# Performance work log

Hardware: AMD Instinct MI355X
Metric: run time of the kernel (lower is better)

## Reference

```python
import jax, jax.numpy as jnp
import numpy as np

TEMPERATURE = 0.07
SCALE_BY_TEMPERATURE = True
N = 4096
D = 256
N_POS = 32768
CHUNK = 128  # row-chunk size for the cdist to bound the [CHUNK, N, D] temp


def setup_inputs() -> dict:
    key = jax.random.key(0)
    k1, k2, k3 = jax.random.split(key, 3)
    out = jax.random.normal(k1, (N, D), dtype=jnp.float32)
    row = jax.random.randint(k2, (N_POS,), 0, N, dtype=jnp.int32)
    col = jax.random.randint(k3, (N_POS,), 0, N, dtype=jnp.int32)
    return {"out": out, "row": row, "col": col}


def _l1_cdist(x):
    """Pairwise Manhattan distance [N, N], computed in row chunks so the
    [CHUNK, N, D] broadcast temporary stays bounded."""
    n, d = x.shape
    xr = x.reshape(n // CHUNK, CHUNK, d)

    def chunk_dist(xc):  # xc: [CHUNK, D] -> [CHUNK, N]
        return jnp.sum(jnp.abs(xc[:, None, :] - x[None, :, :]), axis=-1)

    return jax.lax.map(chunk_dist, xr).reshape(n, n)


def reference(out, row, col):
    n = out.shape[0]
    sim = -_l1_cdist(out) / TEMPERATURE                      # [N, N]
    logits_max = jax.lax.stop_gradient(jnp.max(sim, axis=1, keepdims=True))
    sim = sim - logits_max
    logits_mask = 1.0 - jnp.eye(n, dtype=sim.dtype)          # zero out self-sims
    denom = jnp.log(jnp.sum(jnp.exp(sim) * logits_mask, axis=1, keepdims=True))
    log_probs = sim - denom                                  # [N, N]
    loss = -jnp.mean(log_probs[row, col])                    # gather positive pairs
    if SCALE_BY_TEMPERATURE:
        loss = loss * TEMPERATURE
    return loss
```

## Files before the change

kernel.cpp:

```cpp
#include <hip/hip_runtime.h>
#include <math.h>

#define N 4096
#define D 256
#define NPOS 32768
#define TEMP 0.07f
#define INVT (1.0f / 0.07f)
#define BIGF 3.0e38f

#define RQ 5.5f
#define QS (255.0f / (2.0f * RQ))
#define DEQ (2.0f * RQ / 255.0f)

#define NT 64
#define NTRI (NT * (NT + 1) / 2)
#define KC 16
#define LP 68

#define WS_PSTAT 0
#define WS_T    (2 * N * NT)
#define WS_ACC  (2 * N * NT + N)
#define WS_CNT  (2 * N * NT + N + 1)
#define WS_XQ   (2 * N * NT + N + 4)

__device__ __forceinline__ void sad_acc(unsigned a, unsigned b, unsigned& c) {
#if __has_builtin(__builtin_amdgcn_sad_u8)
    c = __builtin_amdgcn_sad_u8(a, b, c);
#else
    asm("v_sad_u8 %0, %1, %2, %0" : "+v"(c) : "v"(a), "v"(b));
#endif
}

__device__ __forceinline__ unsigned quant1(float v) {
    const float f = fminf(fmaxf((v + RQ) * QS, 0.0f), 255.0f);
    return (unsigned)__float2uint_rn(f);
}

__global__ __launch_bounds__(256)
void cvt_init_k(const float* __restrict__ x, unsigned* __restrict__ xq,
                float* __restrict__ acc, unsigned* __restrict__ cnt) {
    const int i = blockIdx.x * 256 + threadIdx.x;
    const float4 v = ((const float4*)x)[i];
    const unsigned q = quant1(v.x) | (quant1(v.y) << 8) |
                       (quant1(v.z) << 16) | (quant1(v.w) << 24);
    xq[i] = q;
    if (i == 0) { *acc = 0.0f; *cnt = 0u; }
}

__global__ __launch_bounds__(64, 2)
void dist_tile_k(const unsigned* __restrict__ xq, float2* __restrict__ pstat) {
    const int tt = blockIdx.x;
    const int u_ = (NTRI - 1) - tt;
    int r = (int)((sqrtf((float)(8 * u_ + 1)) - 1.0f) * 0.5f);
    while (r * (r + 1) / 2 > u_) --r;
    while ((r + 1) * (r + 2) / 2 <= u_) ++r;
    const int bm = (NT - 1) - r;
    const int bn = (NT - 1) - (u_ - r * (r + 1) / 2);
    const bool diag = (bm == bn);

    const int lane = threadIdx.x;
    const int tx = lane & 7;
    const int ty = lane >> 3;

    __shared__ unsigned As[KC][LP];
    __shared__ unsigned Bs[KC][LP];

    unsigned uacc[2][2][4][4];
#pragma unroll
    for (int rh = 0; rh < 2; ++rh)
#pragma unroll
        for (int ch = 0; ch < 2; ++ch)
#pragma unroll
            for (int i = 0; i < 4; ++i)
#pragma unroll
                for (int j = 0; j < 4; ++j) uacc[rh][ch][i][j] = 0u;

    const int rowA0 = bm * 64;
    const int rowB0 = bn * 64;

    const int su = lane & 3;
    const int r0 = lane >> 2;
    const uint4* gA = (const uint4*)xq + (size_t)(rowA0 + r0) * 16 + su;
    const uint4* gB = (const uint4*)xq + (size_t)(rowB0 + r0) * 16 + su;

    const int aoff = ty * 4;
    const int boff = tx * 4;

    for (int chk = 0; chk < 4; ++chk) {
        uint4 la[4], lb[4];
#pragma unroll
        for (int c = 0; c < 4; ++c) la[c] = gA[chk * 4 + (size_t)c * 256];
#pragma unroll
        for (int c = 0; c < 4; ++c) lb[c] = gB[chk * 4 + (size_t)c * 256];
        asm volatile("s_waitcnt lgkmcnt(0)" ::: "memory");
#pragma unroll
        for (int c = 0; c < 4; ++c) {
            const int rr = r0 + 16 * c;
            As[su * 4 + 0][rr] = la[c].x; As[su * 4 + 1][rr] = la[c].y;
            As[su * 4 + 2][rr] = la[c].z; As[su * 4 + 3][rr] = la[c].w;
            Bs[su * 4 + 0][rr] = lb[c].x; Bs[su * 4 + 1][rr] = lb[c].y;
            Bs[su * 4 + 2][rr] = lb[c].z; Bs[su * 4 + 3][rr] = lb[c].w;
        }
        asm volatile("s_waitcnt lgkmcnt(0)" ::: "memory");

#pragma unroll
        for (int k4 = 0; k4 < KC; ++k4) {
            const uint4 alo = *(const uint4*)&As[k4][aoff];
            const uint4 ahi = *(const uint4*)&As[k4][aoff + 32];
            const uint4 blo = *(const uint4*)&Bs[k4][boff];
            const uint4 bhi = *(const uint4*)&Bs[k4][boff + 32];
            const unsigned av[2][4] = {{alo.x, alo.y, alo.z, alo.w},
                                       {ahi.x, ahi.y, ahi.z, ahi.w}};
            const unsigned bv[2][4] = {{blo.x, blo.y, blo.z, blo.w},
                                       {bhi.x, bhi.y, bhi.z, bhi.w}};
#pragma unroll
            for (int rh = 0; rh < 2; ++rh)
#pragma unroll
                for (int chq = 0; chq < 2; ++chq)
#pragma unroll
                    for (int i = 0; i < 4; ++i)
#pragma unroll
                        for (int j = 0; j < 4; ++j)
                            sad_acc(av[rh][i], bv[chq][j], uacc[rh][chq][i][j]);
        }
    }

    float acc[2][2][4][4];
#pragma unroll
    for (int rh = 0; rh < 2; ++rh)
#pragma unroll
        for (int chq = 0; chq < 2; ++chq)
#pragma unroll
            for (int i = 0; i < 4; ++i)
#pragma unroll
                for (int j = 0; j < 4; ++j)
                    acc[rh][chq][i][j] = (float)uacc[rh][chq][i][j] * DEQ;

    if (diag) {
#pragma unroll
        for (int rh = 0; rh < 2; ++rh)
#pragma unroll
            for (int chq = 0; chq < 2; ++chq)
#pragma unroll
                for (int i = 0; i < 4; ++i)
#pragma unroll
                    for (int j = 0; j < 4; ++j)
                        if (rh * 32 + ty * 4 + i == chq * 32 + tx * 4 + j)
                            acc[rh][chq][i][j] = BIGF;
    }

#pragma unroll
    for (int rh = 0; rh < 2; ++rh) {
#pragma unroll
        for (int i = 0; i < 4; ++i) {
            float mn = BIGF;
#pragma unroll
            for (int chq = 0; chq < 2; ++chq)
#pragma unroll
                for (int j = 0; j < 4; ++j) mn = fminf(mn, acc[rh][chq][i][j]);
            mn = fminf(mn, __shfl_xor(mn, 1, 64));
            mn = fminf(mn, __shfl_xor(mn, 2, 64));
            mn = fminf(mn, __shfl_xor(mn, 4, 64));
            float s = 0.0f;
#pragma unroll
            for (int chq = 0; chq < 2; ++chq)
#pragma unroll
                for (int j = 0; j < 4; ++j)
                    s += __expf((mn - acc[rh][chq][i][j]) * INVT);
            s += __shfl_xor(s, 1, 64);
            s += __shfl_xor(s, 2, 64);
            s += __shfl_xor(s, 4, 64);
            if (tx == 0)
                pstat[(size_t)(rowA0 + rh * 32 + ty * 4 + i) * NT + bn] =
                    make_float2(mn, s);
        }
    }

    if (!diag) {
#pragma unroll
        for (int chq = 0; chq < 2; ++chq) {
#pragma unroll
            for (int j = 0; j < 4; ++j) {
                float mn = BIGF;
#pragma unroll
                for (int rh = 0; rh < 2; ++rh)
#pragma unroll
                    for (int i = 0; i < 4; ++i) mn = fminf(mn, acc[rh][chq][i][j]);
                mn = fminf(mn, __shfl_xor(mn, 8, 64));
                mn = fminf(mn, __shfl_xor(mn, 16, 64));
                mn = fminf(mn, __shfl_xor(mn, 32, 64));
                float s = 0.0f;
#pragma unroll
                for (int rh = 0; rh < 2; ++rh)
#pragma unroll
                    for (int i = 0; i < 4; ++i)
                        s += __expf((mn - acc[rh][chq][i][j]) * INVT);
                s += __shfl_xor(s, 8, 64);
                s += __shfl_xor(s, 16, 64);
                s += __shfl_xor(s, 32, 64);
                if (ty == 0)
                    pstat[(size_t)(rowB0 + chq * 32 + tx * 4 + j) * NT + bm] =
                        make_float2(mn, s);
            }
        }
    }
}

__global__ __launch_bounds__(256)
void row_stats_k(const float2* __restrict__ pstat, float* __restrict__ t) {
    const int r = blockIdx.x * 4 + (threadIdx.x >> 6);
    const int c = threadIdx.x & 63;
    const float2 p = pstat[(size_t)r * NT + c];
    float mn = p.x;
#pragma unroll
    for (int off = 32; off > 0; off >>= 1) mn = fminf(mn, __shfl_xor(mn, off, 64));
    float s = p.y * __expf((mn - p.x) * INVT);
#pragma unroll
    for (int off = 32; off > 0; off >>= 1) s += __shfl_xor(s, off, 64);
    if (c == 0) t[r] = TEMP * __logf(s) - mn;
}

__global__ __launch_bounds__(256)
void pair_fin_k(const float* __restrict__ x, const int* __restrict__ row,
                const int* __restrict__ col, const float* __restrict__ t,
                float* __restrict__ acc, unsigned* __restrict__ cnt,
                float* __restrict__ out) {
    const int lane = threadIdx.x & 63;
    const int wave = threadIdx.x >> 6;
    const int p0 = (blockIdx.x * 4 + wave) * 8;

    int rp[8], cp[8];
#pragma unroll
    for (int i = 0; i < 8; ++i) { rp[i] = row[p0 + i]; cp[i] = col[p0 + i]; }
    float4 a[8], b[8];
#pragma unroll
    for (int i = 0; i < 8; ++i) {
        a[i] = *(const float4*)&x[(size_t)rp[i] * D + lane * 4];
        b[i] = *(const float4*)&x[(size_t)cp[i] * D + lane * 4];
    }
    float wsum = 0.0f;
#pragma unroll
    for (int i = 0; i < 8; ++i) {
        float d = fabsf(a[i].x - b[i].x) + fabsf(a[i].y - b[i].y) +
                  fabsf(a[i].z - b[i].z) + fabsf(a[i].w - b[i].w);
#pragma unroll
        for (int off = 32; off > 0; off >>= 1) d += __shfl_xor(d, off, 64);
        if (lane == 0) wsum += d + t[rp[i]];
    }

    __shared__ float bs[4];
    if (lane == 0) bs[wave] = wsum;
    __syncthreads();
    if (threadIdx.x == 0) {
        const float tot = bs[0] + bs[1] + bs[2] + bs[3];
        atomicAdd(acc, tot);
        __threadfence();
        const unsigned tk = atomicAdd(cnt, 1u);
        if (tk == (unsigned)(gridDim.x - 1)) {
            const float v = atomicAdd(acc, 0.0f);
            out[0] = v * (1.0f / (float)NPOS);
        }
    }
}

extern "C" void kernel_launch(void* const* d_in, const int* in_sizes, int n_in,
                              void* d_out, int out_size, void* d_ws, size_t ws_size,
                              hipStream_t stream) {
    const float* x = (const float*)d_in[0];
    const int* row = (const int*)d_in[1];
    const int* col = (const int*)d_in[2];
    float* ws = (float*)d_ws;
    float* out = (float*)d_out;
    unsigned* xq = (unsigned*)(ws + WS_XQ);
    float* acc = ws + WS_ACC;
    unsigned* cnt = (unsigned*)(ws + WS_CNT);

    cvt_init_k<<<(N * D / 4) / 256, 256, 0, stream>>>(x, xq, acc, cnt);

    dist_tile_k<<<NTRI, 64, 0, stream>>>(xq, (float2*)(ws + WS_PSTAT));

    row_stats_k<<<N / 4, 256, 0, stream>>>((const float2*)(ws + WS_PSTAT), ws + WS_T);

    pair_fin_k<<<NPOS / 32, 256, 0, stream>>>(x, row, col, ws + WS_T, acc, cnt, out);
}
```

Measured before the change: 132.1 us.

## Split each 64x64 distance tile across two wavefronts with shared-memory row-stat merge

Each distance tile is now handled by a 128-thread block of two wavefronts. Each wave computes half of the tile's columns, so per-thread accumulators are halved and more waves can be resident per CU. The row min and sum-of-exp from the two waves are merged through shared memory before being written out. The price is __syncthreads barriers around every LDS staging step plus an extra merge pass, and the A-tile LDS reads are now duplicated across both waves.

Result: faster. 125.4 us, median of 2 (-5.0%).

```diff
diff --git a/kernel.cpp b/kernel.cpp
--- a/kernel.cpp
+++ b/kernel.cpp
@@ -47,7 +47,7 @@
     if (i == 0) { *acc = 0.0f; *cnt = 0u; }
 }
 
-__global__ __launch_bounds__(64, 2)
+__global__ __launch_bounds__(128, 4)
 void dist_tile_k(const unsigned* __restrict__ xq, float2* __restrict__ pstat) {
     const int tt = blockIdx.x;
     const int u_ = (NTRI - 1) - tt;
@@ -58,95 +58,89 @@
     const int bn = (NT - 1) - (u_ - r * (r + 1) / 2);
     const bool diag = (bm == bn);
 
-    const int lane = threadIdx.x;
+    const int tid = threadIdx.x;
+    const int lane = tid & 63;
+    const int w = tid >> 6;
     const int tx = lane & 7;
     const int ty = lane >> 3;
 
     __shared__ unsigned As[KC][LP];
     __shared__ unsigned Bs[KC][LP];
-
-    unsigned uacc[2][2][4][4];
+    __shared__ float rmin_s[2][64];
+    __shared__ float rsum_s[2][64];
+
+    unsigned uacc[2][4][4];
 #pragma unroll
     for (int rh = 0; rh < 2; ++rh)
 #pragma unroll
-        for (int ch = 0; ch < 2; ++ch)
-#pragma unroll
-            for (int i = 0; i < 4; ++i)
-#pragma unroll
-                for (int j = 0; j < 4; ++j) uacc[rh][ch][i][j] = 0u;
+        for (int i = 0; i < 4; ++i)
+#pragma unroll
+            for (int j = 0; j < 4; ++j) uacc[rh][i][j] = 0u;
 
     const int rowA0 = bm * 64;
     const int rowB0 = bn * 64;
 
-    const int su = lane & 3;
-    const int r0 = lane >> 2;
-    const uint4* gA = (const uint4*)xq + (size_t)(rowA0 + r0) * 16 + su;
-    const uint4* gB = (const uint4*)xq + (size_t)(rowB0 + r0) * 16 + su;
-
-    const int aoff = ty * 4;
-    const int boff = tx * 4;
+    const int sr = tid >> 2;
+    const int su = tid & 3;
+    const uint4* gA0 = (const uint4*)xq + (size_t)(rowA0 + sr) * 16 + su;
+    const uint4* gA1 = (const uint4*)xq + (size_t)(rowA0 + sr + 32) * 16 + su;
+    const uint4* gB0 = (const uint4*)xq + (size_t)(rowB0 + sr) * 16 + su;
+    const uint4* gB1 = (const uint4*)xq + (size_t)(rowB0 + sr + 32) * 16 + su;
+
+    const int boff = w * 32 + tx * 4;
 
     for (int chk = 0; chk < 4; ++chk) {
-        uint4 la[4], lb[4];
-#pragma unroll
-        for (int c = 0; c < 4; ++c) la[c] = gA[chk * 4 + (size_t)c * 256];
-#pragma unroll
-        for (int c = 0; c < 4; ++c) lb[c] = gB[chk * 4 + (size_t)c * 256];
-        asm volatile("s_waitcnt lgkmcnt(0)" ::: "memory");
-#pragma unroll
-        for (int c = 0; c < 4; ++c) {
-            const int rr = r0 + 16 * c;
-            As[su * 4 + 0][rr] = la[c].x; As[su * 4 + 1][rr] = la[c].y;
-            As[su * 4 + 2][rr] = la[c].z; As[su * 4 + 3][rr] = la[c].w;
-            Bs[su * 4 + 0][rr] = lb[c].x; Bs[su * 4 + 1][rr] = lb[c].y;
-            Bs[su * 4 + 2][rr] = lb[c].z; Bs[su * 4 + 3][rr] = lb[c].w;
-        }
-        asm volatile("s_waitcnt lgkmcnt(0)" ::: "memory");
+        const uint4 la0 = gA0[chk * 4];
+        const uint4 la1 = gA1[chk * 4];
+        const uint4 lb0 = gB0[chk * 4];
+        const uint4 lb1 = gB1[chk * 4];
+        __syncthreads();
+        As[su * 4 + 0][sr] = la0.x; As[su * 4 + 1][sr] = la0.y;
+        As[su * 4 + 2][sr] = la0.z; As[su * 4 + 3][sr] = la0.w;
+        As[su * 4 + 0][sr + 32] = la1.x; As[su * 4 + 1][sr + 32] = la1.y;
+        As[su * 4 + 2][sr + 32] = la1.z; As[su * 4 + 3][sr + 32] = la1.w;
+        Bs[su * 4 + 0][sr] = lb0.x; Bs[su * 4 + 1][sr] = lb0.y;
+        Bs[su * 4 + 2][sr] = lb0.z; Bs[su * 4 + 3][sr] = lb0.w;
+        Bs[su * 4 + 0][sr + 32] = lb1.x; Bs[su * 4 + 1][sr + 32] = lb1.y;
+        Bs[su * 4 + 2][sr + 32] = lb1.z; Bs[su * 4 + 3][sr + 32] = lb1.w;
+        __syncthreads();
 
 #pragma unroll
         for (int k4 = 0; k4 < KC; ++k4) {
-            const uint4 alo = *(const uint4*)&As[k4][aoff];
-            const uint4 ahi = *(const uint4*)&As[k4][aoff + 32];
-            const uint4 blo = *(const uint4*)&Bs[k4][boff];
-            const uint4 bhi = *(const uint4*)&Bs[k4][boff + 32];
+            const uint4 alo = *(const uint4*)&As[k4][ty * 4];
+            const uint4 ahi = *(const uint4*)&As[k4][32 + ty * 4];
+            const uint4 bw = *(const uint4*)&Bs[k4][boff];
             const unsigned av[2][4] = {{alo.x, alo.y, alo.z, alo.w},
                                        {ahi.x, ahi.y, ahi.z, ahi.w}};
-            const unsigned bv[2][4] = {{blo.x, blo.y, blo.z, blo.w},
-                                       {bhi.x, bhi.y, bhi.z, bhi.w}};
+            const unsigned bv[4] = {bw.x, bw.y, bw.z, bw.w};
 #pragma unroll
             for (int rh = 0; rh < 2; ++rh)
 #pragma unroll
-                for (int chq = 0; chq < 2; ++chq)
-#pragma unroll
-                    for (int i = 0; i < 4; ++i)
-#pragma unroll
-                        for (int j = 0; j < 4; ++j)
-                            sad_acc(av[rh][i], bv[chq][j], uacc[rh][chq][i][j]);
-        }
-    }
-
-    float acc[2][2][4][4];
+                for (int i = 0; i < 4; ++i)
+#pragma unroll
+                    for (int j = 0; j < 4; ++j)
+                        sad_acc(av[rh][i], bv[j], uacc[rh][i][j]);
+        }
+    }
+
+    float acc[2][4][4];
 #pragma unroll
     for (int rh = 0; rh < 2; ++rh)
 #pragma unroll
-        for (int chq = 0; chq < 2; ++chq)
+        for (int i = 0; i < 4; ++i)
+#pragma unroll
+            for (int j = 0; j < 4; ++j)
+                acc[rh][i][j] = (float)uacc[rh][i][j] * DEQ;
+
+    if (diag) {
+#pragma unroll
+        for (int rh = 0; rh < 2; ++rh)
 #pragma unroll
             for (int i = 0; i < 4; ++i)
 #pragma unroll
                 for (int j = 0; j < 4; ++j)
-                    acc[rh][chq][i][j] = (float)uacc[rh][chq][i][j] * DEQ;
-
-    if (diag) {
-#pragma unroll
-        for (int rh = 0; rh < 2; ++rh)
-#pragma unroll
-            for (int chq = 0; chq < 2; ++chq)
-#pragma unroll
-                for (int i = 0; i < 4; ++i)
-#pragma unroll
-                    for (int j = 0; j < 4; ++j)
-                        if (rh * 32 + ty * 4 + i == chq * 32 + tx * 4 + j)
-                            acc[rh][chq][i][j] = BIGF;
+                    if (rh * 32 + ty * 4 + i == w * 32 + tx * 4 + j)
+                        acc[rh][i][j] = BIGF;
     }
 
 #pragma unroll
@@ -155,54 +149,57 @@
         for (int i = 0; i < 4; ++i) {
             float mn = BIGF;
 #pragma unroll
-            for (int chq = 0; chq < 2; ++chq)
-#pragma unroll
-                for (int j = 0; j < 4; ++j) mn = fminf(mn, acc[rh][chq][i][j]);
+            for (int j = 0; j < 4; ++j) mn = fminf(mn, acc[rh][i][j]);
             mn = fminf(mn, __shfl_xor(mn, 1, 64));
             mn = fminf(mn, __shfl_xor(mn, 2, 64));
             mn = fminf(mn, __shfl_xor(mn, 4, 64));
             float s = 0.0f;
 #pragma unroll
-            for (int chq = 0; chq < 2; ++chq)
-#pragma unroll
-                for (int j = 0; j < 4; ++j)
-                    s += __expf((mn - acc[rh][chq][i][j]) * INVT);
+            for (int j = 0; j < 4; ++j)
+                s += __expf((mn - acc[rh][i][j]) * INVT);
             s += __shfl_xor(s, 1, 64);
             s += __shfl_xor(s, 2, 64);
             s += __shfl_xor(s, 4, 64);
-            if (tx == 0)
-                pstat[(size_t)(rowA0 + rh * 32 + ty * 4 + i) * NT + bn] =
+            if (tx == 0) {
+                rmin_s[w][rh * 32 + ty * 4 + i] = mn;
+                rsum_s[w][rh * 32 + ty * 4 + i] = s;
+            }
+        }
+    }
+
+    if (!diag) {
+#pragma unroll
+        for (int j = 0; j < 4; ++j) {
+            float mn = BIGF;
+#pragma unroll
+            for (int rh = 0; rh < 2; ++rh)
+#pragma unroll
+                for (int i = 0; i < 4; ++i) mn = fminf(mn, acc[rh][i][j]);
+            mn = fminf(mn, __shfl_xor(mn, 8, 64));
+            mn = fminf(mn, __shfl_xor(mn, 16, 64));
+            mn = fminf(mn, __shfl_xor(mn, 32, 64));
+            float s = 0.0f;
+#pragma unroll
+            for (int rh = 0; rh < 2; ++rh)
+#pragma unroll
+                for (int i = 0; i < 4; ++i)
+                    s += __expf((mn - acc[rh][i][j]) * INVT);
+            s += __shfl_xor(s, 8, 64);
+            s += __shfl_xor(s, 16, 64);
+            s += __shfl_xor(s, 32, 64);
+            if (ty == 0)
+                pstat[(size_t)(rowB0 + w * 32 + tx * 4 + j) * NT + bm] =
                     make_float2(mn, s);
         }
     }
 
-    if (!diag) {
-#pragma unroll
-        for (int chq = 0; chq < 2; ++chq) {
-#pragma unroll
-            for (int j = 0; j < 4; ++j) {
-                float mn = BIGF;
-#pragma unroll
-                for (int rh = 0; rh < 2; ++rh)
-#pragma unroll
-                    for (int i = 0; i < 4; ++i) mn = fminf(mn, acc[rh][chq][i][j]);
-                mn = fminf(mn, __shfl_xor(mn, 8, 64));
-                mn = fminf(mn, __shfl_xor(mn, 16, 64));
-                mn = fminf(mn, __shfl_xor(mn, 32, 64));
-                float s = 0.0f;
-#pragma unroll
-                for (int rh = 0; rh < 2; ++rh)
-#pragma unroll
-                    for (int i = 0; i < 4; ++i)
-                        s += __expf((mn - acc[rh][chq][i][j]) * INVT);
-                s += __shfl_xor(s, 8, 64);
-                s += __shfl_xor(s, 16, 64);
-                s += __shfl_xor(s, 32, 64);
-                if (ty == 0)
-                    pstat[(size_t)(rowB0 + chq * 32 + tx * 4 + j) * NT + bm] =
-                        make_float2(mn, s);
-            }
-        }
+    __syncthreads();
+    if (tid < 64) {
+        const float m0 = rmin_s[0][tid], m1 = rmin_s[1][tid];
+        const float mn = fminf(m0, m1);
+        const float s = rsum_s[0][tid] * __expf((mn - m0) * INVT) +
+                        rsum_s[1][tid] * __expf((mn - m1) * INVT);
+        pstat[(size_t)(rowA0 + tid) * NT + bn] = make_float2(mn, s);
     }
 }
 
@@ -277,7 +274,7 @@
 
     cvt_init_k<<<(N * D / 4) / 256, 256, 0, stream>>>(x, xq, acc, cnt);
 
-    dist_tile_k<<<NTRI, 64, 0, stream>>>(xq, (float2*)(ws + WS_PSTAT));
+    dist_tile_k<<<NTRI, 128, 0, stream>>>(xq, (float2*)(ws + WS_PSTAT));
 
     row_stats_k<<<N / 4, 256, 0, stream>>>((const float2*)(ws + WS_PSTAT), ws + WS_T);
 
```

## Split K dimension across two waves per tile with LDS reduction

Applied to the files above, without the earlier changes.

The distance tile kernel now runs 128 threads per block. Each of the two wavefronts handles half of the K chunk's SAD accumulation, and the partial sums are reduced through a shared-memory buffer before wave 0 does the epilogue. The aim is more waves in flight and shorter per-wave latency for the 64x64 tiles, since the triangular grid has only about 2080 blocks. The cost is extra barriers, an 8KB LDS reduction buffer, and an idle second wave during the epilogue.

Result: faster. 126.9 us (-3.9%).

```diff
diff --git a/kernel.cpp b/kernel.cpp
--- a/kernel.cpp
+++ b/kernel.cpp
@@ -47,7 +47,7 @@
     if (i == 0) { *acc = 0.0f; *cnt = 0u; }
 }
 
-__global__ __launch_bounds__(64, 2)
+__global__ __launch_bounds__(128, 4)
 void dist_tile_k(const unsigned* __restrict__ xq, float2* __restrict__ pstat) {
     const int tt = blockIdx.x;
     const int u_ = (NTRI - 1) - tt;
@@ -58,12 +58,15 @@
     const int bn = (NT - 1) - (u_ - r * (r + 1) / 2);
     const bool diag = (bm == bn);
 
-    const int lane = threadIdx.x;
+    const int tid = threadIdx.x;
+    const int lane = tid & 63;
+    const int w = tid >> 6;
     const int tx = lane & 7;
     const int ty = lane >> 3;
 
     __shared__ unsigned As[KC][LP];
     __shared__ unsigned Bs[KC][LP];
+    __shared__ unsigned mbuf[2048];
 
     unsigned uacc[2][2][4][4];
 #pragma unroll
@@ -78,33 +81,36 @@
     const int rowA0 = bm * 64;
     const int rowB0 = bn * 64;
 
-    const int su = lane & 3;
-    const int r0 = lane >> 2;
-    const uint4* gA = (const uint4*)xq + (size_t)(rowA0 + r0) * 16 + su;
-    const uint4* gB = (const uint4*)xq + (size_t)(rowB0 + r0) * 16 + su;
+    const int sr = tid >> 2;
+    const int su = tid & 3;
+    const uint4* gA0 = (const uint4*)xq + (size_t)(rowA0 + sr) * 16 + su;
+    const uint4* gA1 = (const uint4*)xq + (size_t)(rowA0 + sr + 32) * 16 + su;
+    const uint4* gB0 = (const uint4*)xq + (size_t)(rowB0 + sr) * 16 + su;
+    const uint4* gB1 = (const uint4*)xq + (size_t)(rowB0 + sr + 32) * 16 + su;
 
     const int aoff = ty * 4;
     const int boff = tx * 4;
+    const int kbase = w * 8;
 
     for (int chk = 0; chk < 4; ++chk) {
-        uint4 la[4], lb[4];
-#pragma unroll
-        for (int c = 0; c < 4; ++c) la[c] = gA[chk * 4 + (size_t)c * 256];
-#pragma unroll
-        for (int c = 0; c < 4; ++c) lb[c] = gB[chk * 4 + (size_t)c * 256];
-        asm volatile("s_waitcnt lgkmcnt(0)" ::: "memory");
-#pragma unroll
-        for (int c = 0; c < 4; ++c) {
-            const int rr = r0 + 16 * c;
-            As[su * 4 + 0][rr] = la[c].x; As[su * 4 + 1][rr] = la[c].y;
-            As[su * 4 + 2][rr] = la[c].z; As[su * 4 + 3][rr] = la[c].w;
-            Bs[su * 4 + 0][rr] = lb[c].x; Bs[su * 4 + 1][rr] = lb[c].y;
-            Bs[su * 4 + 2][rr] = lb[c].z; Bs[su * 4 + 3][rr] = lb[c].w;
-        }
-        asm volatile("s_waitcnt lgkmcnt(0)" ::: "memory");
-
-#pragma unroll
-        for (int k4 = 0; k4 < KC; ++k4) {
+        const uint4 la0 = gA0[chk * 4];
+        const uint4 la1 = gA1[chk * 4];
+        const uint4 lb0 = gB0[chk * 4];
+        const uint4 lb1 = gB1[chk * 4];
+        __syncthreads();
+        As[su * 4 + 0][sr] = la0.x; As[su * 4 + 1][sr] = la0.y;
+        As[su * 4 + 2][sr] = la0.z; As[su * 4 + 3][sr] = la0.w;
+        As[su * 4 + 0][sr + 32] = la1.x; As[su * 4 + 1][sr + 32] = la1.y;
+        As[su * 4 + 2][sr + 32] = la1.z; As[su * 4 + 3][sr + 32] = la1.w;
+        Bs[su * 4 + 0][sr] = lb0.x; Bs[su * 4 + 1][sr] = lb0.y;
+        Bs[su * 4 + 2][sr] = lb0.z; Bs[su * 4 + 3][sr] = lb0.w;
+        Bs[su * 4 + 0][sr + 32] = lb1.x; Bs[su * 4 + 1][sr + 32] = lb1.y;
+        Bs[su * 4 + 2][sr + 32] = lb1.z; Bs[su * 4 + 3][sr + 32] = lb1.w;
+        __syncthreads();
+
+#pragma unroll
+        for (int kk = 0; kk < 8; ++kk) {
+            const int k4 = kbase + kk;
             const uint4 alo = *(const uint4*)&As[k4][aoff];
             const uint4 ahi = *(const uint4*)&As[k4][aoff + 32];
             const uint4 blo = *(const uint4*)&Bs[k4][boff];
@@ -124,6 +130,30 @@
                             sad_acc(av[rh][i], bv[chq][j], uacc[rh][chq][i][j]);
         }
     }
+
+    unsigned* fl = &uacc[0][0][0][0];
+#pragma unroll
+    for (int ph = 0; ph < 2; ++ph) {
+        __syncthreads();
+        if (w == 1) {
+#pragma unroll
+            for (int g = 0; g < 8; ++g)
+                *(uint4*)&mbuf[lane * 4 + g * 256] =
+                    make_uint4(fl[ph * 32 + g * 4 + 0], fl[ph * 32 + g * 4 + 1],
+                               fl[ph * 32 + g * 4 + 2], fl[ph * 32 + g * 4 + 3]);
+        }
+        __syncthreads();
+        if (w == 0) {
+#pragma unroll
+            for (int g = 0; g < 8; ++g) {
+                const uint4 v = *(const uint4*)&mbuf[lane * 4 + g * 256];
+                fl[ph * 32 + g * 4 + 0] += v.x; fl[ph * 32 + g * 4 + 1] += v.y;
+                fl[ph * 32 + g * 4 + 2] += v.z; fl[ph * 32 + g * 4 + 3] += v.w;
+            }
+        }
+    }
+
+    if (w != 0) return;
 
     float acc[2][2][4][4];
 #pragma unroll
@@ -277,7 +307,7 @@
 
     cvt_init_k<<<(N * D / 4) / 256, 256, 0, stream>>>(x, xq, acc, cnt);
 
-    dist_tile_k<<<NTRI, 64, 0, stream>>>(xq, (float2*)(ws + WS_PSTAT));
+    dist_tile_k<<<NTRI, 128, 0, stream>>>(xq, (float2*)(ws + WS_PSTAT));
 
     row_stats_k<<<N / 4, 256, 0, stream>>>((const float2*)(ws + WS_PSTAT), ws + WS_T);
 
```
